# Performance work log

Hardware: AMD Instinct MI355X
Metric: run time of the kernel (lower is better)

The kernel has to match this reference:

```python
import jax, jax.numpy as jnp
import numpy as np

B, S, IN, D, H, K, NLVL = 8, 1536, 32, 128, 4, 7, 2
DFF = 4 * D
DK = D // H
EPS = 1e-6


def setup_inputs() -> dict:
    key = jax.random.key(0)
    ks = jax.random.split(key, 24)
    rn = lambda k, sh, s=0.05: jax.random.normal(k, sh, jnp.float32) * s
    z = lambda sh: jnp.zeros(sh, jnp.float32)
    o = lambda sh: jnp.ones(sh, jnp.float32)
    return {
        'x': jax.random.normal(ks[0], (B, S, IN), jnp.float32),
        'enc_W': rn(ks[1], (IN, D)), 'enc_b': z((D,)),
        'ln_rnn_a': o((NLVL, D)), 'ln_rnn_b': z((NLVL, D)),
        'gru_Wih': rn(ks[2], (NLVL, 3 * D, D)), 'gru_Whh': rn(ks[3], (NLVL, 3 * D, D)),
        'gru_bih': z((NLVL, 3 * D)), 'gru_bhh': z((NLVL, 3 * D)),
        'ln_attn_a': o((NLVL, D)), 'ln_attn_b': z((NLVL, D)),
        'Wq': rn(ks[4], (NLVL, D, D)), 'bq': z((NLVL, D)),
        'Wk': rn(ks[5], (NLVL, D, D)), 'bk': z((NLVL, D)),
        'Wv': rn(ks[6], (NLVL, D, D)), 'bv': z((NLVL, D)),
        'Wo': rn(ks[7], (NLVL, D, D)), 'bo': z((NLVL, D)),
        'ln_ff_a': o((NLVL, D)), 'ln_ff_b': z((NLVL, D)),
        'ff_W1': rn(ks[8], (NLVL, D, DFF)), 'ff_b1': z((NLVL, DFF)),
        'ff_W2': rn(ks[9], (NLVL, DFF, D)), 'ff_b2': z((NLVL, D)),
        'out_W': rn(ks[10], (D, 1)), 'out_b': z((1,)),
    }


def layernorm(x, a, b):
    # faithful to torch code: unbiased std (ddof=1), divide by (std + eps)
    m = x.mean(-1, keepdims=True)
    s = jnp.std(x, axis=-1, ddof=1, keepdims=True)
    return a * (x - m) / (s + EPS) + b


def local_rnn(x, Wih, Whh, bih, bhh):
    # x: [B,S,D]. Window each position into its ksize-length causal window,
    # run a GRU over the window (scan over K steps, batched over B*S), keep last h.
    xp = jnp.pad(x, ((0, 0), (K - 1, 0), (0, 0)))            # zero left-pad
    win = jnp.stack([xp[:, i:i + S] for i in range(K)], 0)   # [K,B,S,D]

    def step(h, xt):
        gi = xt @ Wih.T + bih                                 # [B,S,3D]
        gh = h @ Whh.T + bhh
        ir, iz, inn = jnp.split(gi, 3, -1)
        hr, hz, hn = jnp.split(gh, 3, -1)
        r = jax.nn.sigmoid(ir + hr)
        zz = jax.nn.sigmoid(iz + hz)
        nn_ = jnp.tanh(inn + r * hn)
        return (1.0 - zz) * nn_ + zz * h, None

    h, _ = jax.lax.scan(step, jnp.zeros_like(x), win)
    return h


def mhpool(x, Wq, bq, Wk, bk, Wv, bv, Wo, bo):
    def heads(w, bb):
        return jnp.swapaxes((x @ w + bb).reshape(B, S, H, DK), 1, 2)  # [B,H,S,DK]
    q, k, v = heads(Wq, bq), heads(Wk, bk), heads(Wv, bv)
    scores = jnp.einsum('bhqd,bhkd->bhqk', q, k) / np.float32(np.sqrt(DK))
    mask = jnp.tril(jnp.ones((S, S), bool))
    scores = jnp.where(mask, scores, jnp.float32(-1e9))
    p = jax.nn.softmax(scores, axis=-1)
    o = jnp.einsum('bhqk,bhkd->bhqd', p, v)
    o = jnp.swapaxes(o, 1, 2).reshape(B, S, D)
    return o @ Wo + bo


def reference(x, enc_W, enc_b, ln_rnn_a, ln_rnn_b, gru_Wih, gru_Whh, gru_bih,
              gru_bhh, ln_attn_a, ln_attn_b, Wq, bq, Wk, bk, Wv, bv, Wo, bo,
              ln_ff_a, ln_ff_b, ff_W1, ff_b1, ff_W2, ff_b2, out_W, out_b):
    h = x @ enc_W + enc_b
    for i in range(NLVL):
        # LocalRNNLayer (pre-norm residual); LocalRNN.output Linear is unused in orig forward
        h = h + local_rnn(layernorm(h, ln_rnn_a[i], ln_rnn_b[i]),
                          gru_Wih[i], gru_Whh[i], gru_bih[i], gru_bhh[i])
        # MHPooling sublayer
        h = h + mhpool(layernorm(h, ln_attn_a[i], ln_attn_b[i]),
                       Wq[i], bq[i], Wk[i], bk[i], Wv[i], bv[i], Wo[i], bo[i])
        # PositionwiseFeedForward sublayer
        hn = layernorm(h, ln_ff_a[i], ln_ff_b[i])
        h = h + (jax.nn.relu(hn @ ff_W1[i] + ff_b1[i]) @ ff_W2[i] + ff_b2[i])
    return jax.nn.sigmoid(h @ out_W + out_b)
```

## Files before the change

kernel.cpp:

```cpp
#include <hip/hip_runtime.h>
#include <math.h>

#define DEV_INLINE __device__ __forceinline__

constexpr int B = 8, S = 1536, IN = 32, D = 128, NH = 4, KWIN = 7, NLVL = 2;
constexpr int DFF = 512, DKH = 32;
constexpr int M = B * S;
constexpr int MD = M * D;
constexpr float EPS = 1e-6f;

typedef unsigned short u16;
typedef __bf16 bf16x8 __attribute__((ext_vector_type(8)));
typedef float f32x4 __attribute__((ext_vector_type(4)));
typedef unsigned short u16x4 __attribute__((ext_vector_type(4)));

#define MFMA16(a, b, c) __builtin_amdgcn_mfma_f32_16x16x32_bf16(a, b, c, 0, 0, 0)

DEV_INLINE float sigmoidf_(float x) { return 1.f / (1.f + __expf(-x)); }

DEV_INLINE u16 f2bf(float f) {
    unsigned u = __builtin_bit_cast(unsigned, f);
    unsigned rnd = 0x7FFFu + ((u >> 16) & 1u);
    return (u16)((u + rnd) >> 16);
}
// ... 18 lines not shown
__global__ void k_prep(const float* __restrict__ Wih, const float* __restrict__ Whh,
                       const float* __restrict__ Wq, const float* __restrict__ Wk,
                       const float* __restrict__ Wv, const float* __restrict__ Wo,
                       const float* __restrict__ W1, const float* __restrict__ W2,
                       u16* __restrict__ Wih16, u16* __restrict__ Whh16,
                       u16* __restrict__ Wqkv, u16* __restrict__ WoT,
                       u16* __restrict__ W1T, u16* __restrict__ W2T) {
    constexpr int SZ_GRU = NLVL * 384 * 128;
    constexpr int SZ_DD  = NLVL * 128 * 128;
    constexpr int SZ_FF  = NLVL * 128 * 512;
    int i = blockIdx.x * 256 + threadIdx.x;
    if (i < SZ_GRU) { Wih16[i] = f2bf(Wih[i]); return; }
    i -= SZ_GRU;
    if (i < SZ_GRU) { Whh16[i] = f2bf(Whh[i]); return; }
    i -= SZ_GRU;
    if (i < 3 * SZ_DD) {
        int seg = i / SZ_DD, j = i - seg * SZ_DD;
        int lvl = j >> 14, rem = j & 16383, k = rem >> 7, n = rem & 127;
        const float* src = seg == 0 ? Wq : (seg == 1 ? Wk : Wv);
        Wqkv[(size_t)lvl * 384 * 128 + (size_t)(seg * 128 + n) * 128 + k] = f2bf(src[j]);
        return;
    }
    i -= 3 * SZ_DD;
    if (i < SZ_DD) {
        int lvl = i >> 14, rem = i & 16383, k = rem >> 7, n = rem & 127;
        WoT[(size_t)lvl * 16384 + n * 128 + k] = f2bf(Wo[i]); return;
    }
    i -= SZ_DD;
    if (i < SZ_FF) {
        int lvl = i >> 16, rem = i & 65535, k = rem >> 9, n = rem & 511;
        W1T[(size_t)lvl * 65536 + n * 128 + k] = f2bf(W1[i]); return;
    }
    i -= SZ_FF;
    if (i < SZ_FF) {
        int lvl = i >> 16, rem = i & 65535, k = rem >> 7, n = rem & 127;
        W2T[(size_t)lvl * 65536 + n * 512 + k] = f2bf(W2[i]); return;
    }
}

__global__ __launch_bounds__(256) void k_encoder(
    const float* __restrict__ x, const float* __restrict__ W, const float* __restrict__ b,
    const float* __restrict__ ga, const float* __restrict__ gb,
    float* __restrict__ h, u16* __restrict__ xnout) {
    __shared__ float xs[32][33];
    __shared__ float Ws[32][128];
    const int tid = threadIdx.x;
    const int row0 = blockIdx.x * 32;
    for (int i = tid; i < 32 * 32; i += 256) xs[i >> 5][i & 31] = x[(size_t)row0 * IN + i];
    for (int i = tid; i < 32 * 128; i += 256) Ws[i >> 7][i & 127] = W[i];
    __syncthreads();
    const int r = tid >> 3, cg = (tid & 7) * 16;
    float acc[16];
    #pragma unroll
    for (int j = 0; j < 16; ++j) acc[j] = b[cg + j];
    for (int k = 0; k < IN; ++k) {
        const float xv = xs[r][k];
        #pragma unroll
        for (int j = 0; j < 16; ++j) acc[j] = fmaf(xv, Ws[k][cg + j], acc[j]);
    }
    float s = 0.f;
    #pragma unroll
    for (int j = 0; j < 16; ++j) s += acc[j];
    s += __shfl_xor(s, 1); s += __shfl_xor(s, 2); s += __shfl_xor(s, 4);
    const float mean = s * (1.f / D);
    float q = 0.f;
    #pragma unroll
    for (int j = 0; j < 16; ++j) { float d = acc[j] - mean; q += d * d; }
    q += __shfl_xor(q, 1); q += __shfl_xor(q, 2); q += __shfl_xor(q, 4);
    const float inv = 1.f / (sqrtf(q * (1.f / (D - 1))) + EPS);
    float* hp = h + (size_t)(row0 + r) * D + cg;
    u16* xp = xnout + (size_t)(row0 + r) * D + cg;
    #pragma unroll
    for (int jj = 0; jj < 4; ++jj) {
        float4 hv = make_float4(acc[4 * jj], acc[4 * jj + 1], acc[4 * jj + 2], acc[4 * jj + 3]);
        *(float4*)(hp + 4 * jj) = hv;
        u16x4 o;
        #pragma unroll
        for (int c = 0; c < 4; ++c)
            o[c] = f2bf(ga[cg + 4 * jj + c] * (acc[4 * jj + c] - mean) * inv + gb[cg + 4 * jj + c]);
        *(u16x4*)(xp + 4 * jj) = o;
    }
}

template <int KDIM>
__global__ __launch_bounds__(256) void k_gemm_mfma(
    const u16* __restrict__ A, const u16* __restrict__ Bt,
    const float* __restrict__ bias, u16* __restrict__ o16, int Ncols) {
    const int wave = threadIdx.x >> 6, lane = threadIdx.x & 63;
    const int col16 = lane & 15, quad = lane >> 4;
    const int row0 = (blockIdx.x * 4 + wave) * 32;
    const int c0 = blockIdx.y * 32;
    const u16* a0p = A + (size_t)(row0 + col16) * KDIM + quad * 8;
    const u16* b0p = Bt + (size_t)(c0 + col16) * KDIM + quad * 8;
    f32x4 acc00 = {0.f, 0.f, 0.f, 0.f}, acc01 = acc00, acc10 = acc00, acc11 = acc00;
    mfma_tile32<KDIM>(a0p, a0p + 16 * KDIM, b0p, b0p + 16 * KDIM, acc00, acc01, acc10, acc11);
    const float bv0 = bias ? bias[c0 + col16] : 0.f;
    const float bv1 = bias ? bias[c0 + 16 + col16] : 0.f;
    #pragma unroll
    for (int r = 0; r < 4; ++r) {
        const size_t r0 = (size_t)(row0 + quad * 4 + r) * Ncols;
        const size_t r1 = r0 + (size_t)16 * Ncols;
        o16[r0 + c0 + col16]      = f2bf(acc00[r] + bv0);
        o16[r0 + c0 + 16 + col16] = f2bf(acc01[r] + bv1);
        o16[r1 + c0 + col16]      = f2bf(acc10[r] + bv0);
        o16[r1 + c0 + 16 + col16] = f2bf(acc11[r] + bv1);
    }
}

__global__ __launch_bounds__(256) void k_gemm_qkv(
    const u16* __restrict__ A, const u16* __restrict__ Bqkv,
    const float* __restrict__ bq, const float* __restrict__ bk, const float* __restrict__ bv,
    u16* __restrict__ q16, u16* __restrict__ k16, u16* __restrict__ vt16) {
    constexpr float QS = 0.17677669529663687f * 1.4426950408889634f;
    const int wave = threadIdx.x >> 6, lane = threadIdx.x & 63;
    const int col16 = lane & 15, quad = lane >> 4;
    const int row0 = (blockIdx.x * 4 + wave) * 32;
    const int seg = blockIdx.y >> 2;
    const int c0 = (blockIdx.y & 3) * 32;
    const u16* a0p = A + (size_t)(row0 + col16) * 128 + quad * 8;
    const u16* b0p = Bqkv + (size_t)(seg * 128 + c0 + col16) * 128 + quad * 8;
    f32x4 acc00 = {0.f, 0.f, 0.f, 0.f}, acc01 = acc00, acc10 = acc00, acc11 = acc00;
    mfma_tile32<128>(a0p, a0p + 16 * 128, b0p, b0p + 16 * 128, acc00, acc01, acc10, acc11);
    const float* bias = seg == 0 ? bq : (seg == 1 ? bk : bv);
    const float bv0 = bias[c0 + col16];
    const float bv1 = bias[c0 + 16 + col16];
    if (seg < 2) {
        const float sc = seg == 0 ? QS : 1.f;
        u16* o16 = seg == 0 ? q16 : k16;
        #pragma unroll
        for (int r = 0; r < 4; ++r) {
            const size_t r0 = (size_t)(row0 + quad * 4 + r) * 128;
            const size_t r1 = r0 + 16 * 128;
            o16[r0 + c0 + col16]      = f2bf((acc00[r] + bv0) * sc);
            o16[r0 + c0 + 16 + col16] = f2bf((acc01[r] + bv1) * sc);
            o16[r1 + c0 + col16]      = f2bf((acc10[r] + bv0) * sc);
            o16[r1 + c0 + 16 + col16] = f2bf((acc11[r] + bv1) * sc);
        }
    } else {
        const int bb = row0 / S;
        const int ssv = row0 - bb * S;
        const int ca = c0 + col16, cb = c0 + 16 + col16;
        u16* pa = vt16 + ((size_t)((bb * NH + (ca >> 5)) * 32 + (ca & 31))) * S + ssv;
        u16* pb = vt16 + ((size_t)((bb * NH + (cb >> 5)) * 32 + (cb & 31))) * S + ssv;
        #pragma unroll
        for (int r = 0; r < 4; ++r) {
            const int lr = quad * 4 + r;
            pa[lr]      = f2bf(acc00[r] + bv0);
            pb[lr]      = f2bf(acc01[r] + bv1);
            pa[lr + 16] = f2bf(acc10[r] + bv0);
            pb[lr + 16] = f2bf(acc11[r] + bv1);
        }
    }
}

template <int KDIM>
__global__ __launch_bounds__(256) void k_gemm_row(
    const u16* __restrict__ A, const u16* __restrict__ Bt,
    const float* __restrict__ bias, float* __restrict__ hio,
    const float* __restrict__ ga, const float* __restrict__ gb,
    u16* __restrict__ xnout) {
    __shared__ float hL[32][132];
    const int wave = threadIdx.x >> 6, lane = threadIdx.x & 63;
    const int col16 = lane & 15, quad = lane >> 4;
    const int row0 = blockIdx.x * 32;
    const int c0 = wave * 32;
    const u16* a0p = A + (size_t)(row0 + col16) * KDIM + quad * 8;
    const u16* b0p = Bt + (size_t)(c0 + col16) * KDIM + quad * 8;
    f32x4 acc00 = {0.f, 0.f, 0.f, 0.f}, acc01 = acc00, acc10 = acc00, acc11 = acc00;
    mfma_tile32<KDIM>(a0p, a0p + 16 * KDIM, b0p, b0p + 16 * KDIM, acc00, acc01, acc10, acc11);
    const float bv0 = bias[c0 + col16];
    const float bv1 = bias[c0 + 16 + col16];
    #pragma unroll
    for (int r = 0; r < 4; ++r) {
        const int l0 = quad * 4 + r, l1 = 16 + quad * 4 + r;
        const size_t g0 = (size_t)(row0 + l0) * D, g1 = (size_t)(row0 + l1) * D;
        float v00 = acc00[r] + bv0 + hio[g0 + c0 + col16];
        float v01 = acc01[r] + bv1 + hio[g0 + c0 + 16 + col16];
        float v10 = acc10[r] + bv0 + hio[g1 + c0 + col16];
        float v11 = acc11[r] + bv1 + hio[g1 + c0 + 16 + col16];
        hio[g0 + c0 + col16]      = v00;  hL[l0][c0 + col16]      = v00;
        hio[g0 + c0 + 16 + col16] = v01;  hL[l0][c0 + 16 + col16] = v01;
        hio[g1 + c0 + col16]      = v10;  hL[l1][c0 + col16]      = v10;
        hio[g1 + c0 + 16 + col16] = v11;  hL[l1][c0 + 16 + col16] = v11;
    }
    __syncthreads();
    const int r = threadIdx.x >> 3, cg = (threadIdx.x & 7) * 16;
    float vals[16];
    #pragma unroll
    for (int jj = 0; jj < 4; ++jj) {
        float4 v = *(const float4*)&hL[r][cg + 4 * jj];
        vals[4 * jj] = v.x; vals[4 * jj + 1] = v.y; vals[4 * jj + 2] = v.z; vals[4 * jj + 3] = v.w;
    }
    float s = 0.f;
    #pragma unroll
    for (int j = 0; j < 16; ++j) s += vals[j];
    s += __shfl_xor(s, 1); s += __shfl_xor(s, 2); s += __shfl_xor(s, 4);
    const float mean = s * (1.f / D);
    float q = 0.f;
    #pragma unroll
    for (int j = 0; j < 16; ++j) { float d = vals[j] - mean; q += d * d; }
    q += __shfl_xor(q, 1); q += __shfl_xor(q, 2); q += __shfl_xor(q, 4);
    const float inv = 1.f / (sqrtf(q * (1.f / (D - 1))) + EPS);
    u16* xp = xnout + (size_t)(row0 + r) * D + cg;
    #pragma unroll
    for (int jj = 0; jj < 4; ++jj) {
        u16x4 o;
        #pragma unroll
        for (int c = 0; c < 4; ++c)
            o[c] = f2bf(ga[cg + 4 * jj + c] * (vals[4 * jj + c] - mean) * inv + gb[cg + 4 * jj + c]);
        *(u16x4*)(xp + 4 * jj) = o;
    }
}

template <bool LAST>
__global__ __launch_bounds__(256) void k_ffn(
    const u16* __restrict__ A, const u16* __restrict__ W1T, const float* __restrict__ b1,
    const u16* __restrict__ W2T, const float* __restrict__ b2, float* __restrict__ hio,
    const float* __restrict__ ga, const float* __restrict__ gb, u16* __restrict__ xnout,
    const float* __restrict__ outW, const float* __restrict__ outb, float* __restrict__ outp) {
    __shared__ __align__(16) u16 Ls[32][520];
    const int tid = threadIdx.x;
    const int wave = tid >> 6, lane = tid & 63;
    const int col16 = lane & 15, quad = lane >> 4;
    const int row0 = blockIdx.x * 32;
    const u16* a0p = A + (size_t)(row0 + col16) * 128 + quad * 8;
    const u16* a1p = a0p + 16 * 128;

    #pragma unroll
    for (int ct = 0; ct < 4; ++ct) {
        const int c0 = wave * 128 + ct * 32;
        const u16* b0p = W1T + (size_t)(c0 + col16) * 128 + quad * 8;
        f32x4 acc00 = {0.f, 0.f, 0.f, 0.f}, acc01 = acc00, acc10 = acc00, acc11 = acc00;
        mfma_tile32<128>(a0p, a1p, b0p, b0p + 16 * 128, acc00, acc01, acc10, acc11);
        const float bv0 = b1[c0 + col16];
        const float bv1 = b1[c0 + 16 + col16];
        #pragma unroll
        for (int r = 0; r < 4; ++r) {
            const int l0 = quad * 4 + r, l1 = 16 + quad * 4 + r;
            Ls[l0][c0 + col16]      = f2bf(fmaxf(acc00[r] + bv0, 0.f));
            Ls[l0][c0 + 16 + col16] = f2bf(fmaxf(acc01[r] + bv1, 0.f));
            Ls[l1][c0 + col16]      = f2bf(fmaxf(acc10[r] + bv0, 0.f));
            Ls[l1][c0 + 16 + col16] = f2bf(fmaxf(acc11[r] + bv1, 0.f));
        }
    }
    __syncthreads();

    const int c0 = wave * 32;
    f32x4 acc00 = {0.f, 0.f, 0.f, 0.f}, acc01 = acc00, acc10 = acc00, acc11 = acc00;
    #pragma unroll
    for (int k0 = 0; k0 < 512; k0 += 32) {
        bf16x8 a0 = *(const bf16x8*)&Ls[col16][k0 + quad * 8];
        bf16x8 a1 = *(const bf16x8*)&Ls[16 + col16][k0 + quad * 8];
        const u16* bp = W2T + (size_t)(c0 + col16) * 512 + k0 + quad * 8;
        bf16x8 b0 = *(const bf16x8*)bp;
        bf16x8 b1v = *(const bf16x8*)(bp + 16 * 512);
        acc00 = MFMA16(a0, b0, acc00);
        acc01 = MFMA16(a0, b1v, acc01);
        acc10 = MFMA16(a1, b0, acc10);
        acc11 = MFMA16(a1, b1v, acc11);
    }
    __syncthreads();
    float* hL = (float*)Ls;
    const float bv0 = b2[c0 + col16];
    const float bv1 = b2[c0 + 16 + col16];
    #pragma unroll
    for (int r = 0; r < 4; ++r) {
        const int l0 = quad * 4 + r, l1 = 16 + quad * 4 + r;
        const size_t g0 = (size_t)(row0 + l0) * D, g1 = (size_t)(row0 + l1) * D;
        float v00 = acc00[r] + bv0 + hio[g0 + c0 + col16];
        float v01 = acc01[r] + bv1 + hio[g0 + c0 + 16 + col16];
        float v10 = acc10[r] + bv0 + hio[g1 + c0 + col16];
        float v11 = acc11[r] + bv1 + hio[g1 + c0 + 16 + col16];
        hio[g0 + c0 + col16]      = v00;  hL[l0 * 132 + c0 + col16]      = v00;
        hio[g0 + c0 + 16 + col16] = v01;  hL[l0 * 132 + c0 + 16 + col16] = v01;
        hio[g1 + c0 + col16]      = v10;  hL[l1 * 132 + c0 + col16]      = v10;
        hio[g1 + c0 + 16 + col16] = v11;  hL[l1 * 132 + c0 + 16 + col16] = v11;
    }
    __syncthreads();
    const int r = tid >> 3, cg = (tid & 7) * 16;
    float vals[16];
    #pragma unroll
    for (int jj = 0; jj < 4; ++jj) {
        float4 v = *(const float4*)&hL[r * 132 + cg + 4 * jj];
        vals[4 * jj] = v.x; vals[4 * jj + 1] = v.y; vals[4 * jj + 2] = v.z; vals[4 * jj + 3] = v.w;
    }
    if constexpr (LAST) {
        float dot = 0.f;
        #pragma unroll
        for (int j = 0; j < 16; ++j) dot += vals[j] * outW[cg + j];
        dot += __shfl_xor(dot, 1); dot += __shfl_xor(dot, 2); dot += __shfl_xor(dot, 4);
        if ((tid & 7) == 0) outp[row0 + r] = sigmoidf_(dot + outb[0]);
    } else {
        float s = 0.f;
        #pragma unroll
        for (int j = 0; j < 16; ++j) s += vals[j];
        s += __shfl_xor(s, 1); s += __shfl_xor(s, 2); s += __shfl_xor(s, 4);
        const float mean = s * (1.f / D);
        float q = 0.f;
        #pragma unroll
        for (int j = 0; j < 16; ++j) { float d = vals[j] - mean; q += d * d; }
        q += __shfl_xor(q, 1); q += __shfl_xor(q, 2); q += __shfl_xor(q, 4);
        const float inv = 1.f / (sqrtf(q * (1.f / (D - 1))) + EPS);
        u16* xp = xnout + (size_t)(row0 + r) * D + cg;
        #pragma unroll
        for (int jj = 0; jj < 4; ++jj) {
            u16x4 o;
            #pragma unroll
            for (int c = 0; c < 4; ++c)
                o[c] = f2bf(ga[cg + 4 * jj + c] * (vals[4 * jj + c] - mean) * inv + gb[cg + 4 * jj + c]);
            *(u16x4*)(xp + 4 * jj) = o;
        }
    }
}

__global__ __launch_bounds__(512, 2) void k_gru_fused(
    const u16* __restrict__ Gb,
    const u16* __restrict__ Whh16,
    const float* __restrict__ bih, const float* __restrict__ bhh,
    float* __restrict__ hout,
    const float* __restrict__ ga, const float* __restrict__ gb,
    u16* __restrict__ xnout) {
    constexpr int RB = 48;
    __shared__ __align__(16) u16 Gs[(RB + 6) * 392];
    __shared__ __align__(16) u16 hs16[RB * 136];
    const int tid = threadIdx.x;
    const int wave = tid >> 6, lane = tid & 63;
    const int col16 = lane & 15, quad = lane >> 4;
    const int row0 = blockIdx.x * RB;
    const int ss0 = row0 % S;
    const int cc = wave * 16 + col16;

    for (int i = tid; i < (RB + 6) * 48; i += 512) {
        const int r = i / 48, c8 = (i - r * 48) * 8;
        bf16x8 val = {};
        if (ss0 - 6 + r >= 0)
            val = *(const bf16x8*)(Gb + (size_t)(row0 - 6 + r) * 384 + c8);
        *(bf16x8*)&Gs[r * 392 + c8] = val;
    }
    bf16x8 Breg[3][4];
    #pragma unroll
    for (int g = 0; g < 3; ++g)
        #pragma unroll
        for (int kc = 0; kc < 4; ++kc)
            Breg[g][kc] = *(const bf16x8*)(Whh16 + (size_t)(g * 128 + cc) * 128 + kc * 32 + quad * 8);
    float bi[3], bh[3];
    #pragma unroll
    for (int g = 0; g < 3; ++g) { bi[g] = bih[g * 128 + cc]; bh[g] = bhh[g * 128 + cc]; }
    float hp[12] = {};
    __syncthreads();

    for (int t = 0; t < KWIN; ++t) {
        const int shift = KWIN - 1 - t;
        f32x4 acc[3][3];
        #pragma unroll
        for (int rh = 0; rh < 3; ++rh)
            #pragma unroll
            for (int g = 0; g < 3; ++g) acc[rh][g] = {0.f, 0.f, 0.f, 0.f};
        if (t > 0) {
            bf16x8 af[3][4];
            #pragma unroll
            for (int rh = 0; rh < 3; ++rh)
                #pragma unroll
                for (int kc = 0; kc < 4; ++kc)
                    af[rh][kc] = *(const bf16x8*)&hs16[(rh * 16 + col16) * 136 + kc * 32 + quad * 8];
            __syncthreads();
            #pragma unroll
            for (int kc = 0; kc < 4; ++kc)
                #pragma unroll
                for (int g = 0; g < 3; ++g)
                    #pragma unroll
                    for (int rh = 0; rh < 3; ++rh)
                        acc[rh][g] = MFMA16(af[rh][kc], Breg[g][kc], acc[rh][g]);
        }
        const bool last = (t == KWIN - 1);
        #pragma unroll
        for (int rh = 0; rh < 3; ++rh) {
            #pragma unroll
            for (int r = 0; r < 4; ++r) {
                const int idx = rh * 4 + r;
                const int lrow = rh * 16 + quad * 4 + r;
                const int gr = lrow - shift + 6;
                float xr = 0.f, xz = 0.f, xn_ = 0.f;
                if (ss0 + lrow - shift >= 0) {
                    xr  = b2f(Gs[gr * 392 + cc]);
                    xz  = b2f(Gs[gr * 392 + 128 + cc]);
                    xn_ = b2f(Gs[gr * 392 + 256 + cc]);
                }
                const float rr = sigmoidf_(xr + bi[0] + acc[rh][0][r] + bh[0]);
                const float zz = sigmoidf_(xz + bi[1] + acc[rh][1][r] + bh[1]);
                const float e2 = __expf(2.f * (xn_ + bi[2] + rr * (acc[rh][2][r] + bh[2])));
                const float nn = 1.f - 2.f / (e2 + 1.f);
                const float hnew = (1.f - zz) * nn + zz * hp[idx];
                hp[idx] = hnew;
                if (!last) hs16[lrow * 136 + cc] = f2bf(hnew);
            }
        }
        __syncthreads();
    }
    float* hf = (float*)Gs;
    #pragma unroll
    for (int rh = 0; rh < 3; ++rh)
        #pragma unroll
        for (int r = 0; r < 4; ++r) {
            const int lrow = rh * 16 + quad * 4 + r;
            const float hv = hp[rh * 4 + r] + hout[(size_t)(row0 + lrow) * D + cc];
            hout[(size_t)(row0 + lrow) * D + cc] = hv;
            hf[lrow * 132 + cc] = hv;
        }
    __syncthreads();
    const int r = tid >> 3;
    if (r < RB) {
        const int cg = (tid & 7) * 16;
        float vals[16];
        #pragma unroll
        for (int jj = 0; jj < 4; ++jj) {
            float4 v = *(const float4*)&hf[r * 132 + cg + 4 * jj];
            vals[4 * jj] = v.x; vals[4 * jj + 1] = v.y; vals[4 * jj + 2] = v.z; vals[4 * jj + 3] = v.w;
        }
        float s = 0.f;
        #pragma unroll
        for (int j = 0; j < 16; ++j) s += vals[j];
        s += __shfl_xor(s, 1); s += __shfl_xor(s, 2); s += __shfl_xor(s, 4);
        const float mean = s * (1.f / D);
        float q = 0.f;
        #pragma unroll
        for (int j = 0; j < 16; ++j) { float d = vals[j] - mean; q += d * d; }
        q += __shfl_xor(q, 1); q += __shfl_xor(q, 2); q += __shfl_xor(q, 4);
        const float inv = 1.f / (sqrtf(q * (1.f / (D - 1))) + EPS);
        u16* xp = xnout + (size_t)(row0 + r) * D + cg;
        #pragma unroll
        for (int jj = 0; jj < 4; ++jj) {
            u16x4 o;
            #pragma unroll
            for (int c = 0; c < 4; ++c)
                o[c] = f2bf(ga[cg + 4 * jj + c] * (vals[4 * jj + c] - mean) * inv + gb[cg + 4 * jj + c]);
            *(u16x4*)(xp + 4 * jj) = o;
        }
    }
}

__global__ __launch_bounds__(256) void k_attn_mfma(
    const u16* __restrict__ Qb, const u16* __restrict__ Kb,
    const u16* __restrict__ Vt, u16* __restrict__ O16) {
    const int wave = threadIdx.x >> 6, lane = threadIdx.x & 63;
    const int p = blockIdx.x;
    const int bh = blockIdx.y;
    const int b = bh >> 2, hh = bh & 3;
    const int col = lane & 15, quad = lane >> 4;

    __shared__ __align__(16) u16 Pb[4][32][40];
    __shared__ float Om[4][32][33];
    __shared__ float Lm[4][32];
    u16 (* __restrict__ P)[40] = Pb[wave];

    const u16* Kbase = Kb + (size_t)b * S * 128 + hh * 32;
    const u16* Vbase = Vt + (size_t)bh * 32 * S;

    #pragma unroll
    for (int half = 0; half < 2; ++half) {
        const int qt = half == 0 ? p : 47 - p;
        const int q0 = qt * 32;
        const int nkt = qt + 1;
        const u16* qp = Qb + (size_t)(b * S + q0 + col) * 128 + hh * 32 + quad * 8;
        const bf16x8 qf0 = *(const bf16x8*)qp;
        const bf16x8 qf1 = *(const bf16x8*)(qp + 16 * 128);
        f32x4 o00 = {0.f, 0.f, 0.f, 0.f}, o01 = o00, o10 = o00, o11 = o00;
        float lsum[8] = {};
        int kt = wave;
        bf16x8 kf0 = {}, kf1 = {}, vf0 = {}, vf1 = {};
        if (kt < nkt) {
            const u16* kp = Kbase + (size_t)(kt * 32 + col) * 128 + quad * 8;
            kf0 = *(const bf16x8*)kp;
            kf1 = *(const bf16x8*)(kp + 16 * 128);
            const u16* vp = Vbase + (size_t)col * S + kt * 32 + quad * 8;
            vf0 = *(const bf16x8*)vp;
            vf1 = *(const bf16x8*)(vp + 16 * S);
        }
        while (kt < nkt) {
            const int ktn = kt + 4;
            bf16x8 nk0 = kf0, nk1 = kf1, nv0 = vf0, nv1 = vf1;
            if (ktn < nkt) {
                const u16* kp = Kbase + (size_t)(ktn * 32 + col) * 128 + quad * 8;
                nk0 = *(const bf16x8*)kp;
                nk1 = *(const bf16x8*)(kp + 16 * 128);
                const u16* vp = Vbase + (size_t)col * S + ktn * 32 + quad * 8;
                nv0 = *(const bf16x8*)vp;
                nv1 = *(const bf16x8*)(vp + 16 * S);
            }
            f32x4 z = {0.f, 0.f, 0.f, 0.f};
            f32x4 s00 = MFMA16(qf0, kf0, z);
            f32x4 s01 = MFMA16(qf0, kf1, z);
            f32x4 s10 = MFMA16(qf1, kf0, z);
            f32x4 s11 = MFMA16(qf1, kf1, z);
            const bool diag = (kt == qt);
            const int k0g = kt * 32;
            #pragma unroll
            for (int r = 0; r < 4; ++r) {
                const int lr = quad * 4 + r;
                float p00 = __builtin_amdgcn_exp2f(s00[r]);
                float p01 = __builtin_amdgcn_exp2f(s01[r]);
                float p10 = __builtin_amdgcn_exp2f(s10[r]);
                float p11 = __builtin_amdgcn_exp2f(s11[r]);
                if (diag) {
                    const int qg0 = q0 + lr, qg1 = q0 + 16 + lr;
                    if (k0g + col > qg0)      p00 = 0.f;
                    if (k0g + 16 + col > qg0) p01 = 0.f;
                    if (k0g + col > qg1)      p10 = 0.f;
                    if (k0g + 16 + col > qg1) p11 = 0.f;
                }
                lsum[r]     += p00 + p01;
                lsum[4 + r] += p10 + p11;
                P[lr][col]           = f2bf(p00);
                P[lr][16 + col]      = f2bf(p01);
                P[16 + lr][col]      = f2bf(p10);
                P[16 + lr][16 + col] = f2bf(p11);
            }
            const bf16x8 pa0 = *(const bf16x8*)&P[col][quad * 8];
            const bf16x8 pa1 = *(const bf16x8*)&P[16 + col][quad * 8];
            o00 = MFMA16(pa0, vf0, o00);
            o01 = MFMA16(pa0, vf1, o01);
            o10 = MFMA16(pa1, vf0, o10);
            o11 = MFMA16(pa1, vf1, o11);
            kf0 = nk0; kf1 = nk1; vf0 = nv0; vf1 = nv1;
            kt = ktn;
        }
        #pragma unroll
        for (int i = 0; i < 8; ++i) {
            float v = lsum[i];
            v += __shfl_xor(v, 1); v += __shfl_xor(v, 2);
            v += __shfl_xor(v, 4); v += __shfl_xor(v, 8);
            lsum[i] = v;
        }
        #pragma unroll
        for (int r = 0; r < 4; ++r) {
            const int lr = quad * 4 + r;
            Om[wave][lr][col]           = o00[r];
            Om[wave][lr][16 + col]      = o01[r];
            Om[wave][16 + lr][col]      = o10[r];
            Om[wave][16 + lr][16 + col] = o11[r];
        }
        if (col == 0) {
            #pragma unroll
            for (int i = 0; i < 8; ++i)
                Lm[wave][(i >> 2) * 16 + quad * 4 + (i & 3)] = lsum[i];
        }
        __syncthreads();
        {
            const int tr = threadIdx.x >> 3, tc = (threadIdx.x & 7) * 4;
            const float inv = 1.f / (Lm[0][tr] + Lm[1][tr] + Lm[2][tr] + Lm[3][tr]);
            u16x4 outv;
            #pragma unroll
            for (int c = 0; c < 4; ++c) {
                const float o = Om[0][tr][tc + c] + Om[1][tr][tc + c] +
                                Om[2][tr][tc + c] + Om[3][tr][tc + c];
                outv[c] = f2bf(o * inv);
            }
            *(u16x4*)(O16 + (size_t)(b * S + q0 + tr) * 128 + hh * 32 + tc) = outv;
        }
        __syncthreads();
    }
}

extern "C" void kernel_launch(void* const* d_in, const int* in_sizes, int n_in,
                              void* d_out, int out_size, void* d_ws, size_t ws_size,
                              hipStream_t stream) {
    const float* x       = (const float*)d_in[0];
    const float* enc_W   = (const float*)d_in[1];
    const float* enc_b   = (const float*)d_in[2];
    const float* ln_rnn_a = (const float*)d_in[3];
    const float* ln_rnn_b = (const float*)d_in[4];
    const float* gru_Wih = (const float*)d_in[5];
    const float* gru_Whh = (const float*)d_in[6];
    const float* gru_bih = (const float*)d_in[7];
    const float* gru_bhh = (const float*)d_in[8];
    const float* ln_attn_a = (const float*)d_in[9];
    const float* ln_attn_b = (const float*)d_in[10];
    const float* Wq = (const float*)d_in[11];
    const float* bq = (const float*)d_in[12];
    const float* Wk = (const float*)d_in[13];
    const float* bk = (const float*)d_in[14];
    const float* Wv = (const float*)d_in[15];
    const float* bv = (const float*)d_in[16];
    const float* Wo = (const float*)d_in[17];
    const float* bo = (const float*)d_in[18];
    const float* ln_ff_a = (const float*)d_in[19];
    const float* ln_ff_b = (const float*)d_in[20];
    const float* ff_W1 = (const float*)d_in[21];
    const float* ff_b1 = (const float*)d_in[22];
    const float* ff_W2 = (const float*)d_in[23];
    const float* ff_b2 = (const float*)d_in[24];
    const float* out_W = (const float*)d_in[25];
    const float* out_b = (const float*)d_in[26];

    float* h   = (float*)d_ws;
    u16* pool  = (u16*)(h + MD);
    u16* xn16  = pool + (size_t)4 * MD;
    u16* Wih16 = xn16 + MD;
    u16* Whh16 = Wih16 + NLVL * 384 * D;
    u16* Wqkv  = Whh16 + NLVL * 384 * D;
    u16* WoT   = Wqkv + NLVL * 384 * D;
    u16* W1T   = WoT + NLVL * D * D;
    u16* W2T   = W1T + NLVL * D * DFF;

    u16* q16  = pool;
    u16* k16  = pool + MD;
    u16* vt16 = pool + (size_t)2 * MD;
    u16* ao16 = pool + (size_t)3 * MD;
    u16* G16  = pool;

    k_prep<<<2304, 256, 0, stream>>>(gru_Wih, gru_Whh, Wq, Wk, Wv, Wo, ff_W1, ff_W2,
                                     Wih16, Whh16, Wqkv, WoT, W1T, W2T);
    k_encoder<<<M / 32, 256, 0, stream>>>(x, enc_W, enc_b, ln_rnn_a, ln_rnn_b, h, xn16);

    for (int lvl = 0; lvl < NLVL; ++lvl) {
        k_gemm_mfma<128><<<dim3(96, 12), 256, 0, stream>>>(
            xn16, Wih16 + lvl * 384 * D, nullptr, G16, 384);
        k_gru_fused<<<256, 512, 0, stream>>>(
            G16, Whh16 + lvl * 384 * D, gru_bih + lvl * 384, gru_bhh + lvl * 384,
            h, ln_attn_a + lvl * D, ln_attn_b + lvl * D, xn16);

        k_gemm_qkv<<<dim3(96, 12), 256, 0, stream>>>(
            xn16, Wqkv + lvl * 384 * D, bq + lvl * D, bk + lvl * D, bv + lvl * D,
            q16, k16, vt16);
        k_attn_mfma<<<dim3(24, 32), 256, 0, stream>>>(q16, k16, vt16, ao16);
        k_gemm_row<128><<<M / 32, 256, 0, stream>>>(
            ao16, WoT + lvl * D * D, bo + lvl * D, h,
            ln_ff_a + lvl * D, ln_ff_b + lvl * D, xn16);

        if (lvl + 1 < NLVL) {
            k_ffn<false><<<M / 32, 256, 0, stream>>>(
                xn16, W1T + lvl * D * DFF, ff_b1 + lvl * DFF,
                W2T + lvl * DFF * D, ff_b2 + lvl * D, h,
                ln_rnn_a + (lvl + 1) * D, ln_rnn_b + (lvl + 1) * D, xn16,
                nullptr, nullptr, nullptr);
        } else {
            k_ffn<true><<<M / 32, 256, 0, stream>>>(
                xn16, W1T + lvl * D * DFF, ff_b1 + lvl * DFF,
                W2T + lvl * DFF * D, ff_b2 + lvl * D, h,
                nullptr, nullptr, nullptr,
                out_W, out_b, (float*)d_out);
        }
    }
}
```

Measured before the change: 360.0 us.

## Fuse GRU input projection into GRU kernel and merge Wo with FFN

The separate Wih GEMM is folded into the GRU kernel. Each block loads its normalized input rows plus a 16-row halo into shared memory and computes the gate preactivations with MFMA there, so the G buffer no longer round-trips through global memory. The output projection with its residual and LayerNorm is merged into the FFN kernel, and the intermediate h stays in shared memory instead of being written and reread. This removes two launches per level and several full-tensor passes through global memory, at the cost of redundant halo GEMM work and more shared memory per block, which may lower occupancy.

```diff
diff --git a/kernel.cpp b/kernel.cpp
--- a/kernel.cpp
+++ b/kernel.cpp
@@ -124,31 +124,6 @@
     }
 }
 
-template <int KDIM>
-__global__ __launch_bounds__(256) void k_gemm_mfma(
-    const u16* __restrict__ A, const u16* __restrict__ Bt,
-    const float* __restrict__ bias, u16* __restrict__ o16, int Ncols) {
-    const int wave = threadIdx.x >> 6, lane = threadIdx.x & 63;
-    const int col16 = lane & 15, quad = lane >> 4;
-    const int row0 = (blockIdx.x * 4 + wave) * 32;
-    const int c0 = blockIdx.y * 32;
-    const u16* a0p = A + (size_t)(row0 + col16) * KDIM + quad * 8;
-    const u16* b0p = Bt + (size_t)(c0 + col16) * KDIM + quad * 8;
-    f32x4 acc00 = {0.f, 0.f, 0.f, 0.f}, acc01 = acc00, acc10 = acc00, acc11 = acc00;
-    mfma_tile32<KDIM>(a0p, a0p + 16 * KDIM, b0p, b0p + 16 * KDIM, acc00, acc01, acc10, acc11);
-    const float bv0 = bias ? bias[c0 + col16] : 0.f;
-    const float bv1 = bias ? bias[c0 + 16 + col16] : 0.f;
-    #pragma unroll
-    for (int r = 0; r < 4; ++r) {
-        const size_t r0 = (size_t)(row0 + quad * 4 + r) * Ncols;
-        const size_t r1 = r0 + (size_t)16 * Ncols;
-        o16[r0 + c0 + col16]      = f2bf(acc00[r] + bv0);
-        o16[r0 + c0 + 16 + col16] = f2bf(acc01[r] + bv1);
-        o16[r1 + c0 + col16]      = f2bf(acc10[r] + bv0);
-        o16[r1 + c0 + 16 + col16] = f2bf(acc11[r] + bv1);
-    }
-}
-
 __global__ __launch_bounds__(256) void k_gemm_qkv(
     const u16* __restrict__ A, const u16* __restrict__ Bqkv,
     const float* __restrict__ bq, const float* __restrict__ bk, const float* __restrict__ bv,
@@ -195,175 +170,17 @@
     }
 }
 
-template <int KDIM>
-__global__ __launch_bounds__(256) void k_gemm_row(
-    const u16* __restrict__ A, const u16* __restrict__ Bt,
-    const float* __restrict__ bias, float* __restrict__ hio,
-    const float* __restrict__ ga, const float* __restrict__ gb,
-    u16* __restrict__ xnout) {
-    __shared__ float hL[32][132];
-    const int wave = threadIdx.x >> 6, lane = threadIdx.x & 63;
-    const int col16 = lane & 15, quad = lane >> 4;
-    const int row0 = blockIdx.x * 32;
-    const int c0 = wave * 32;
-    const u16* a0p = A + (size_t)(row0 + col16) * KDIM + quad * 8;
-    const u16* b0p = Bt + (size_t)(c0 + col16) * KDIM + quad * 8;
-    f32x4 acc00 = {0.f, 0.f, 0.f, 0.f}, acc01 = acc00, acc10 = acc00, acc11 = acc00;
-    mfma_tile32<KDIM>(a0p, a0p + 16 * KDIM, b0p, b0p + 16 * KDIM, acc00, acc01, acc10, acc11);
-    const float bv0 = bias[c0 + col16];
-    const float bv1 = bias[c0 + 16 + col16];
-    #pragma unroll
-    for (int r = 0; r < 4; ++r) {
-        const int l0 = quad * 4 + r, l1 = 16 + quad * 4 + r;
-        const size_t g0 = (size_t)(row0 + l0) * D, g1 = (size_t)(row0 + l1) * D;
-        float v00 = acc00[r] + bv0 + hio[g0 + c0 + col16];
-        float v01 = acc01[r] + bv1 + hio[g0 + c0 + 16 + col16];
-        float v10 = acc10[r] + bv0 + hio[g1 + c0 + col16];
-        float v11 = acc11[r] + bv1 + hio[g1 + c0 + 16 + col16];
-        hio[g0 + c0 + col16]      = v00;  hL[l0][c0 + col16]      = v00;
-        hio[g0 + c0 + 16 + col16] = v01;  hL[l0][c0 + 16 + col16] = v01;
-        hio[g1 + c0 + col16]      = v10;  hL[l1][c0 + col16]      = v10;
-        hio[g1 + c0 + 16 + col16] = v11;  hL[l1][c0 + 16 + col16] = v11;
-    }
-    __syncthreads();
-    const int r = threadIdx.x >> 3, cg = (threadIdx.x & 7) * 16;
-    float vals[16];
-    #pragma unroll
-    for (int jj = 0; jj < 4; ++jj) {
-        float4 v = *(const float4*)&hL[r][cg + 4 * jj];
-        vals[4 * jj] = v.x; vals[4 * jj + 1] = v.y; vals[4 * jj + 2] = v.z; vals[4 * jj + 3] = v.w;
-    }
-    float s = 0.f;
-    #pragma unroll
-    for (int j = 0; j < 16; ++j) s += vals[j];
-    s += __shfl_xor(s, 1); s += __shfl_xor(s, 2); s += __shfl_xor(s, 4);
-    const float mean = s * (1.f / D);
-    float q = 0.f;
-    #pragma unroll
-    for (int j = 0; j < 16; ++j) { float d = vals[j] - mean; q += d * d; }
-    q += __shfl_xor(q, 1); q += __shfl_xor(q, 2); q += __shfl_xor(q, 4);
-    const float inv = 1.f / (sqrtf(q * (1.f / (D - 1))) + EPS);
-    u16* xp = xnout + (size_t)(row0 + r) * D + cg;
-    #pragma unroll
-    for (int jj = 0; jj < 4; ++jj) {
-        u16x4 o;
-        #pragma unroll
-        for (int c = 0; c < 4; ++c)
-            o[c] = f2bf(ga[cg + 4 * jj + c] * (vals[4 * jj + c] - mean) * inv + gb[cg + 4 * jj + c]);
-        *(u16x4*)(xp + 4 * jj) = o;
-    }
-}
-
-template <bool LAST>
-__global__ __launch_bounds__(256) void k_ffn(
-    const u16* __restrict__ A, const u16* __restrict__ W1T, const float* __restrict__ b1,
-    const u16* __restrict__ W2T, const float* __restrict__ b2, float* __restrict__ hio,
-    const float* __restrict__ ga, const float* __restrict__ gb, u16* __restrict__ xnout,
-    const float* __restrict__ outW, const float* __restrict__ outb, float* __restrict__ outp) {
-    __shared__ __align__(16) u16 Ls[32][520];
-    const int tid = threadIdx.x;
-    const int wave = tid >> 6, lane = tid & 63;
-    const int col16 = lane & 15, quad = lane >> 4;
-    const int row0 = blockIdx.x * 32;
-    const u16* a0p = A + (size_t)(row0 + col16) * 128 + quad * 8;
-    const u16* a1p = a0p + 16 * 128;
-
-    #pragma unroll
-    for (int ct = 0; ct < 4; ++ct) {
-        const int c0 = wave * 128 + ct * 32;
-        const u16* b0p = W1T + (size_t)(c0 + col16) * 128 + quad * 8;
-        f32x4 acc00 = {0.f, 0.f, 0.f, 0.f}, acc01 = acc00, acc10 = acc00, acc11 = acc00;
-        mfma_tile32<128>(a0p, a1p, b0p, b0p + 16 * 128, acc00, acc01, acc10, acc11);
-        const float bv0 = b1[c0 + col16];
-        const float bv1 = b1[c0 + 16 + col16];
-        #pragma unroll
-        for (int r = 0; r < 4; ++r) {
-            const int l0 = quad * 4 + r, l1 = 16 + quad * 4 + r;
-            Ls[l0][c0 + col16]      = f2bf(fmaxf(acc00[r] + bv0, 0.f));
-            Ls[l0][c0 + 16 + col16] = f2bf(fmaxf(acc01[r] + bv1, 0.f));
-            Ls[l1][c0 + col16]      = f2bf(fmaxf(acc10[r] + bv0, 0.f));
-            Ls[l1][c0 + 16 + col16] = f2bf(fmaxf(acc11[r] + bv1, 0.f));
-        }
-    }
-    __syncthreads();
-
-    const int c0 = wave * 32;
-    f32x4 acc00 = {0.f, 0.f, 0.f, 0.f}, acc01 = acc00, acc10 = acc00, acc11 = acc00;
-    #pragma unroll
-    for (int k0 = 0; k0 < 512; k0 += 32) {
-        bf16x8 a0 = *(const bf16x8*)&Ls[col16][k0 + quad * 8];
-        bf16x8 a1 = *(const bf16x8*)&Ls[16 + col16][k0 + quad * 8];
-        const u16* bp = W2T + (size_t)(c0 + col16) * 512 + k0 + quad * 8;
-        bf16x8 b0 = *(const bf16x8*)bp;
-        bf16x8 b1v = *(const bf16x8*)(bp + 16 * 512);
-        acc00 = MFMA16(a0, b0, acc00);
-        acc01 = MFMA16(a0, b1v, acc01);
-        acc10 = MFMA16(a1, b0, acc10);
-        acc11 = MFMA16(a1, b1v, acc11);
-    }
-    __syncthreads();
-    float* hL = (float*)Ls;
-    const float bv0 = b2[c0 + col16];
-    const float bv1 = b2[c0 + 16 + col16];
-    #pragma unroll
-    for (int r = 0; r < 4; ++r) {
-        const int l0 = quad * 4 + r, l1 = 16 + quad * 4 + r;
-        const size_t g0 = (size_t)(row0 + l0) * D, g1 = (size_t)(row0 + l1) * D;
-        float v00 = acc00[r] + bv0 + hio[g0 + c0 + col16];
-        float v01 = acc01[r] + bv1 + hio[g0 + c0 + 16 + col16];
-        float v10 = acc10[r] + bv0 + hio[g1 + c0 + col16];
-        float v11 = acc11[r] + bv1 + hio[g1 + c0 + 16 + col16];
-        hio[g0 + c0 + col16]      = v00;  hL[l0 * 132 + c0 + col16]      = v00;
-        hio[g0 + c0 + 16 + col16] = v01;  hL[l0 * 132 + c0 + 16 + col16] = v01;
-        hio[g1 + c0 + col16]      = v10;  hL[l1 * 132 + c0 + col16]      = v10;
-        hio[g1 + c0 + 16 + col16] = v11;  hL[l1 * 132 + c0 + 16 + col16] = v11;
-    }
-    __syncthreads();
-    const int r = tid >> 3, cg = (tid & 7) * 16;
-    float vals[16];
-    #pragma unroll
-    for (int jj = 0; jj < 4; ++jj) {
-        float4 v = *(const float4*)&hL[r * 132 + cg + 4 * jj];
-        vals[4 * jj] = v.x; vals[4 * jj + 1] = v.y; vals[4 * jj + 2] = v.z; vals[4 * jj + 3] = v.w;
-    }
-    if constexpr (LAST) {
-        float dot = 0.f;
-        #pragma unroll
-        for (int j = 0; j < 16; ++j) dot += vals[j] * outW[cg + j];
-        dot += __shfl_xor(dot, 1); dot += __shfl_xor(dot, 2); dot += __shfl_xor(dot, 4);
-        if ((tid & 7) == 0) outp[row0 + r] = sigmoidf_(dot + outb[0]);
-    } else {
-        float s = 0.f;
-        #pragma unroll
-        for (int j = 0; j < 16; ++j) s += vals[j];
-        s += __shfl_xor(s, 1); s += __shfl_xor(s, 2); s += __shfl_xor(s, 4);
-        const float mean = s * (1.f / D);
-        float q = 0.f;
-        #pragma unroll
-        for (int j = 0; j < 16; ++j) { float d = vals[j] - mean; q += d * d; }
-        q += __shfl_xor(q, 1); q += __shfl_xor(q, 2); q += __shfl_xor(q, 4);
-        const float inv = 1.f / (sqrtf(q * (1.f / (D - 1))) + EPS);
-        u16* xp = xnout + (size_t)(row0 + r) * D + cg;
-        #pragma unroll
-        for (int jj = 0; jj < 4; ++jj) {
-            u16x4 o;
-            #pragma unroll
-            for (int c = 0; c < 4; ++c)
-                o[c] = f2bf(ga[cg + 4 * jj + c] * (vals[4 * jj + c] - mean) * inv + gb[cg + 4 * jj + c]);
-            *(u16x4*)(xp + 4 * jj) = o;
-        }
-    }
-}
-
 __global__ __launch_bounds__(512, 2) void k_gru_fused(
-    const u16* __restrict__ Gb,
+    const u16* __restrict__ xn,
+    const u16* __restrict__ Wih16,
     const u16* __restrict__ Whh16,
     const float* __restrict__ bih, const float* __restrict__ bhh,
     float* __restrict__ hout,
     const float* __restrict__ ga, const float* __restrict__ gb,
-    u16* __restrict__ xnout) {
+    u16* __restrict__ xnaout) {
     constexpr int RB = 48;
-    __shared__ __align__(16) u16 Gs[(RB + 6) * 392];
+    __shared__ __align__(16) u16 xnS[64 * 136];
+    __shared__ __align__(16) u16 Gs[64 * 392];
     __shared__ __align__(16) u16 hs16[RB * 136];
     const int tid = threadIdx.x;
     const int wave = tid >> 6, lane = tid & 63;
@@ -372,12 +189,12 @@
     const int ss0 = row0 % S;
     const int cc = wave * 16 + col16;
 
-    for (int i = tid; i < (RB + 6) * 48; i += 512) {
-        const int r = i / 48, c8 = (i - r * 48) * 8;
+    for (int i = tid; i < 64 * 16; i += 512) {
+        const int r = i >> 4, c8 = (i & 15) * 8;
         bf16x8 val = {};
-        if (ss0 - 6 + r >= 0)
-            val = *(const bf16x8*)(Gb + (size_t)(row0 - 6 + r) * 384 + c8);
-        *(bf16x8*)&Gs[r * 392 + c8] = val;
+        if (ss0 - 16 + r >= 0)
+            val = *(const bf16x8*)(xn + (size_t)(row0 - 16 + r) * 128 + c8);
+        *(bf16x8*)&xnS[r * 136 + c8] = val;
     }
     bf16x8 Breg[3][4];
     #pragma unroll
@@ -388,6 +205,33 @@
     float bi[3], bh[3];
     #pragma unroll
     for (int g = 0; g < 3; ++g) { bi[g] = bih[g * 128 + cc]; bh[g] = bhh[g * 128 + cc]; }
+    __syncthreads();
+
+    #pragma unroll
+    for (int tt = wave; tt < 24; tt += 8) {
+        const int rt = tt / 12, ct = tt - rt * 12;
+        const u16* bp = Wih16 + (size_t)(ct * 32 + col16) * 128 + quad * 8;
+        f32x4 a00 = {0.f, 0.f, 0.f, 0.f}, a01 = a00, a10 = a00, a11 = a00;
+        #pragma unroll
+        for (int k0 = 0; k0 < 128; k0 += 32) {
+            bf16x8 af0 = *(const bf16x8*)&xnS[(rt * 32 + col16) * 136 + k0 + quad * 8];
+            bf16x8 af1 = *(const bf16x8*)&xnS[(rt * 32 + 16 + col16) * 136 + k0 + quad * 8];
+            bf16x8 b0 = *(const bf16x8*)(bp + k0);
+            bf16x8 b1 = *(const bf16x8*)(bp + 16 * 128 + k0);
+            a00 = MFMA16(af0, b0, a00);
+            a01 = MFMA16(af0, b1, a01);
+            a10 = MFMA16(af1, b0, a10);
+            a11 = MFMA16(af1, b1, a11);
+        }
+        #pragma unroll
+        for (int r = 0; r < 4; ++r) {
+            const int gr0 = rt * 32 + quad * 4 + r, gr1 = gr0 + 16;
+            Gs[gr0 * 392 + ct * 32 + col16]      = f2bf(a00[r]);
+            Gs[gr0 * 392 + ct * 32 + 16 + col16] = f2bf(a01[r]);
+            Gs[gr1 * 392 + ct * 32 + col16]      = f2bf(a10[r]);
+            Gs[gr1 * 392 + ct * 32 + 16 + col16] = f2bf(a11[r]);
+        }
+    }
     float hp[12] = {};
     __syncthreads();
 
@@ -421,13 +265,10 @@
             for (int r = 0; r < 4; ++r) {
                 const int idx = rh * 4 + r;
                 const int lrow = rh * 16 + quad * 4 + r;
-                const int gr = lrow - shift + 6;
-                float xr = 0.f, xz = 0.f, xn_ = 0.f;
-                if (ss0 + lrow - shift >= 0) {
-                    xr  = b2f(Gs[gr * 392 + cc]);
-                    xz  = b2f(Gs[gr * 392 + 128 + cc]);
-                    xn_ = b2f(Gs[gr * 392 + 256 + cc]);
-                }
+                const int gr = lrow - shift + 16;
+                const float xr  = b2f(Gs[gr * 392 + cc]);
+                const float xz  = b2f(Gs[gr * 392 + 128 + cc]);
+                const float xn_ = b2f(Gs[gr * 392 + 256 + cc]);
                 const float rr = sigmoidf_(xr + bi[0] + acc[rh][0][r] + bh[0]);
                 const float zz = sigmoidf_(xz + bi[1] + acc[rh][1][r] + bh[1]);
                 const float e2 = __expf(2.f * (xn_ + bi[2] + rr * (acc[rh][2][r] + bh[2])));
@@ -469,7 +310,7 @@
         for (int j = 0; j < 16; ++j) { float d = vals[j] - mean; q += d * d; }
         q += __shfl_xor(q, 1); q += __shfl_xor(q, 2); q += __shfl_xor(q, 4);
         const float inv = 1.f / (sqrtf(q * (1.f / (D - 1))) + EPS);
-        u16* xp = xnout + (size_t)(row0 + r) * D + cg;
+        u16* xp = xnaout + (size_t)(row0 + r) * D + cg;
         #pragma unroll
         for (int jj = 0; jj < 4; ++jj) {
             u16x4 o;
@@ -482,8 +323,8 @@
 }
 
 __global__ __launch_bounds__(256) void k_attn_mfma(
-    const u16* __restrict__ Qb, const u16* __restrict__ Kb,
-    const u16* __restrict__ Vt, u16* __restrict__ O16) {
+    const u16* Qb, const u16* __restrict__ Kb,
+    const u16* __restrict__ Vt, u16* O16) {
     const int wave = threadIdx.x >> 6, lane = threadIdx.x & 63;
     const int p = blockIdx.x;
     const int bh = blockIdx.y;
@@ -600,6 +441,171 @@
             *(u16x4*)(O16 + (size_t)(b * S + q0 + tr) * 128 + hh * 32 + tc) = outv;
         }
         __syncthreads();
+    }
+}
+
+template <bool LAST>
+__global__ __launch_bounds__(256) void k_mho_ffn(
+    const u16* __restrict__ ao, const u16* __restrict__ WoT, const float* __restrict__ bo,
+    float* __restrict__ hio,
+    const float* __restrict__ ga1, const float* __restrict__ gb1,
+    const u16* __restrict__ W1T, const float* __restrict__ b1,
+    const u16* __restrict__ W2T, const float* __restrict__ b2,
+    const float* __restrict__ ga2, const float* __restrict__ gb2, u16* __restrict__ xnout,
+    const float* __restrict__ outW, const float* __restrict__ outb, float* __restrict__ outp) {
+    __shared__ float hL[32 * 132];
+    __shared__ __align__(16) u16 xnL[32 * 136];
+    __shared__ __align__(16) u16 Ls[32 * 520];
+    const int tid = threadIdx.x;
+    const int wave = tid >> 6, lane = tid & 63;
+    const int col16 = lane & 15, quad = lane >> 4;
+    const int row0 = blockIdx.x * 32;
+    const int c0 = wave * 32;
+
+    {
+        const u16* a0p = ao + (size_t)(row0 + col16) * 128 + quad * 8;
+        const u16* b0p = WoT + (size_t)(c0 + col16) * 128 + quad * 8;
+        f32x4 acc00 = {0.f, 0.f, 0.f, 0.f}, acc01 = acc00, acc10 = acc00, acc11 = acc00;
+        mfma_tile32<128>(a0p, a0p + 16 * 128, b0p, b0p + 16 * 128, acc00, acc01, acc10, acc11);
+        const float bv0 = bo[c0 + col16];
+        const float bv1 = bo[c0 + 16 + col16];
+        #pragma unroll
+        for (int r = 0; r < 4; ++r) {
+            const int l0 = quad * 4 + r, l1 = 16 + quad * 4 + r;
+            const size_t g0 = (size_t)(row0 + l0) * D, g1 = (size_t)(row0 + l1) * D;
+            hL[l0 * 132 + c0 + col16]      = acc00[r] + bv0 + hio[g0 + c0 + col16];
+            hL[l0 * 132 + c0 + 16 + col16] = acc01[r] + bv1 + hio[g0 + c0 + 16 + col16];
+            hL[l1 * 132 + c0 + col16]      = acc10[r] + bv0 + hio[g1 + c0 + col16];
+            hL[l1 * 132 + c0 + 16 + col16] = acc11[r] + bv1 + hio[g1 + c0 + 16 + col16];
+        }
+    }
+    __syncthreads();
+    {
+        const int r = tid >> 3, cg = (tid & 7) * 16;
+        float vals[16];
+        #pragma unroll
+        for (int jj = 0; jj < 4; ++jj) {
+            float4 v = *(const float4*)&hL[r * 132 + cg + 4 * jj];
+            vals[4 * jj] = v.x; vals[4 * jj + 1] = v.y; vals[4 * jj + 2] = v.z; vals[4 * jj + 3] = v.w;
+        }
+        float s = 0.f;
+        #pragma unroll
+        for (int j = 0; j < 16; ++j) s += vals[j];
+        s += __shfl_xor(s, 1); s += __shfl_xor(s, 2); s += __shfl_xor(s, 4);
+        const float mean = s * (1.f / D);
+        float q = 0.f;
+        #pragma unroll
+        for (int j = 0; j < 16; ++j) { float d = vals[j] - mean; q += d * d; }
+        q += __shfl_xor(q, 1); q += __shfl_xor(q, 2); q += __shfl_xor(q, 4);
+        const float inv = 1.f / (sqrtf(q * (1.f / (D - 1))) + EPS);
+        #pragma unroll
+        for (int jj = 0; jj < 4; ++jj) {
+            u16x4 o;
+            #pragma unroll
+            for (int c = 0; c < 4; ++c)
+                o[c] = f2bf(ga1[cg + 4 * jj + c] * (vals[4 * jj + c] - mean) * inv + gb1[cg + 4 * jj + c]);
+            *(u16x4*)&xnL[r * 136 + cg + 4 * jj] = o;
+        }
+    }
+    __syncthreads();
+    #pragma unroll
+    for (int ct = 0; ct < 4; ++ct) {
+        const int c0f = wave * 128 + ct * 32;
+        const u16* b0p = W1T + (size_t)(c0f + col16) * 128 + quad * 8;
+        f32x4 acc00 = {0.f, 0.f, 0.f, 0.f}, acc01 = acc00, acc10 = acc00, acc11 = acc00;
+        #pragma unroll
+        for (int k0 = 0; k0 < 128; k0 += 32) {
+            bf16x8 a0 = *(const bf16x8*)&xnL[col16 * 136 + k0 + quad * 8];
+            bf16x8 a1 = *(const bf16x8*)&xnL[(16 + col16) * 136 + k0 + quad * 8];
+            bf16x8 b0 = *(const bf16x8*)(b0p + k0);
+            bf16x8 b1 = *(const bf16x8*)(b0p + 16 * 128 + k0);
+            acc00 = MFMA16(a0, b0, acc00);
+            acc01 = MFMA16(a0, b1, acc01);
+            acc10 = MFMA16(a1, b0, acc10);
+            acc11 = MFMA16(a1, b1, acc11);
+        }
+        const float bv0 = b1[c0f + col16];
+        const float bv1 = b1[c0f + 16 + col16];
+        #pragma unroll
+        for (int r = 0; r < 4; ++r) {
+            const int l0 = quad * 4 + r, l1 = 16 + quad * 4 + r;
+            Ls[l0 * 520 + c0f + col16]      = f2bf(fmaxf(acc00[r] + bv0, 0.f));
+            Ls[l0 * 520 + c0f + 16 + col16] = f2bf(fmaxf(acc01[r] + bv1, 0.f));
+            Ls[l1 * 520 + c0f + col16]      = f2bf(fmaxf(acc10[r] + bv0, 0.f));
+            Ls[l1 * 520 + c0f + 16 + col16] = f2bf(fmaxf(acc11[r] + bv1, 0.f));
+        }
+    }
+    __syncthreads();
+    {
+        f32x4 acc00 = {0.f, 0.f, 0.f, 0.f}, acc01 = acc00, acc10 = acc00, acc11 = acc00;
+        #pragma unroll
+        for (int k0 = 0; k0 < 512; k0 += 32) {
+            bf16x8 a0 = *(const bf16x8*)&Ls[col16 * 520 + k0 + quad * 8];
+            bf16x8 a1 = *(const bf16x8*)&Ls[(16 + col16) * 520 + k0 + quad * 8];
+            const u16* bp = W2T + (size_t)(c0 + col16) * 512 + k0 + quad * 8;
+            bf16x8 b0 = *(const bf16x8*)bp;
+            bf16x8 b1v = *(const bf16x8*)(bp + 16 * 512);
+            acc00 = MFMA16(a0, b0, acc00);
+            acc01 = MFMA16(a0, b1v, acc01);
+            acc10 = MFMA16(a1, b0, acc10);
+            acc11 = MFMA16(a1, b1v, acc11);
+        }
+        const float bv0 = b2[c0 + col16];
+        const float bv1 = b2[c0 + 16 + col16];
+        #pragma unroll
+        for (int r = 0; r < 4; ++r) {
+            const int l0 = quad * 4 + r, l1 = 16 + quad * 4 + r;
+            const size_t g0 = (size_t)(row0 + l0) * D, g1 = (size_t)(row0 + l1) * D;
+            const float v00 = acc00[r] + bv0 + hL[l0 * 132 + c0 + col16];
+            const float v01 = acc01[r] + bv1 + hL[l0 * 132 + c0 + 16 + col16];
+            const float v10 = acc10[r] + bv0 + hL[l1 * 132 + c0 + col16];
+            const float v11 = acc11[r] + bv1 + hL[l1 * 132 + c0 + 16 + col16];
+            hio[g0 + c0 + col16]      = v00;
+            hio[g0 + c0 + 16 + col16] = v01;
+            hio[g1 + c0 + col16]      = v10;
+            hio[g1 + c0 + 16 + col16] = v11;
+            hL[l0 * 132 + c0 + col16]      = v00;
+            hL[l0 * 132 + c0 + 16 + col16] = v01;
+            hL[l1 * 132 + c0 + col16]      = v10;
+            hL[l1 * 132 + c0 + 16 + col16] = v11;
+        }
+    }
+    __syncthreads();
+    {
+        const int r = tid >> 3, cg = (tid & 7) * 16;
+        float vals[16];
+        #pragma unroll
+        for (int jj = 0; jj < 4; ++jj) {
+            float4 v = *(const float4*)&hL[r * 132 + cg + 4 * jj];
+            vals[4 * jj] = v.x; vals[4 * jj + 1] = v.y; vals[4 * jj + 2] = v.z; vals[4 * jj + 3] = v.w;
+        }
+        if constexpr (LAST) {
+            float dot = 0.f;
+            #pragma unroll
+            for (int j = 0; j < 16; ++j) dot += vals[j] * outW[cg + j];
+            dot += __shfl_xor(dot, 1); dot += __shfl_xor(dot, 2); dot += __shfl_xor(dot, 4);
+            if ((tid & 7) == 0) outp[row0 + r] = sigmoidf_(dot + outb[0]);
+        } else {
+            float s = 0.f;
+            #pragma unroll
+            for (int j = 0; j < 16; ++j) s += vals[j];
+            s += __shfl_xor(s, 1); s += __shfl_xor(s, 2); s += __shfl_xor(s, 4);
+            const float mean = s * (1.f / D);
+            float q = 0.f;
+            #pragma unroll
+            for (int j = 0; j < 16; ++j) { float d = vals[j] - mean; q += d * d; }
+            q += __shfl_xor(q, 1); q += __shfl_xor(q, 2); q += __shfl_xor(q, 4);
+            const float inv = 1.f / (sqrtf(q * (1.f / (D - 1))) + EPS);
+            u16* xp = xnout + (size_t)(row0 + r) * D + cg;
+            #pragma unroll
+            for (int jj = 0; jj < 4; ++jj) {
+                u16x4 o;
+                #pragma unroll
+                for (int c = 0; c < 4; ++c)
+                    o[c] = f2bf(ga2[cg + 4 * jj + c] * (vals[4 * jj + c] - mean) * inv + gb2[cg + 4 * jj + c]);
+                *(u16x4*)(xp + 4 * jj) = o;
+            }
+        }
     }
 }
 
@@ -644,41 +650,41 @@
     u16* W1T   = WoT + NLVL * D * D;
     u16* W2T   = W1T + NLVL * D * DFF;
 
-    u16* q16  = pool;
-    u16* k16  = pool + MD;
-    u16* vt16 = pool + (size_t)2 * MD;
-    u16* ao16 = pool + (size_t)3 * MD;
-    u16* G16  = pool;
+    u16* q16   = pool;
+    u16* k16   = pool + MD;
+    u16* vt16  = pool + (size_t)2 * MD;
+    u16* xna16 = pool + (size_t)3 * MD;
+    u16* ao16  = q16;
 
     k_prep<<<2304, 256, 0, stream>>>(gru_Wih, gru_Whh, Wq, Wk, Wv, Wo, ff_W1, ff_W2,
                                      Wih16, Whh16, Wqkv, WoT, W1T, W2T);
     k_encoder<<<M / 32, 256, 0, stream>>>(x, enc_W, enc_b, ln_rnn_a, ln_rnn_b, h, xn16);
 
     for (int lvl = 0; lvl < NLVL; ++lvl) {
-        k_gemm_mfma<128><<<dim3(96, 12), 256, 0, stream>>>(
-            xn16, Wih16 + lvl * 384 * D, nullptr, G16, 384);
         k_gru_fused<<<256, 512, 0, stream>>>(
-            G16, Whh16 + lvl * 384 * D, gru_bih + lvl * 384, gru_bhh + lvl * 384,
-            h, ln_attn_a + lvl * D, ln_attn_b + lvl * D, xn16);
+            xn16, Wih16 + lvl * 384 * D, Whh16 + lvl * 384 * D,
+            gru_bih + lvl * 384, gru_bhh + lvl * 384,
+            h, ln_attn_a + lvl * D, ln_attn_b + lvl * D, xna16);
 
         k_gemm_qkv<<<dim3(96, 12), 256, 0, stream>>>(
-            xn16, Wqkv + lvl * 384 * D, bq + lvl * D, bk + lvl * D, bv + lvl * D,
+            xna16, Wqkv + lvl * 384 * D, bq + lvl * D, bk + lvl * D, bv + lvl * D,
             q16, k16, vt16);
         k_attn_mfma<<<dim3(24, 32), 256, 0, stream>>>(q16, k16, vt16, ao16);
-        k_gemm_row<128><<<M / 32, 256, 0, stream>>>(
-            ao16, WoT + lvl * D * D, bo + lvl * D, h,
-            ln_ff_a + lvl * D, ln_ff_b + lvl * D, xn16);
 
         if (lvl + 1 < NLVL) {
-            k_ffn<false><<<M / 32, 256, 0, stream>>>(
-                xn16, W1T + lvl * D * DFF, ff_b1 + lvl * DFF,
-                W2T + lvl * DFF * D, ff_b2 + lvl * D, h,
+            k_mho_ffn<false><<<M / 32, 256, 0, stream>>>(
+                ao16, WoT + lvl * D * D, bo + lvl * D, h,
+                ln_ff_a + lvl * D, ln_ff_b + lvl * D,
+                W1T + lvl * D * DFF, ff_b1 + lvl * DFF,
+                W2T + lvl * DFF * D, ff_b2 + lvl * D,
                 ln_rnn_a + (lvl + 1) * D, ln_rnn_b + (lvl + 1) * D, xn16,
                 nullptr, nullptr, nullptr);
         } else {
-            k_ffn<true><<<M / 32, 256, 0, stream>>>(
-                xn16, W1T + lvl * D * DFF, ff_b1 + lvl * DFF,
-                W2T + lvl * DFF * D, ff_b2 + lvl * D, h,
+            k_mho_ffn<true><<<M / 32, 256, 0, stream>>>(
+                ao16, WoT + lvl * D * D, bo + lvl * D, h,
+                ln_ff_a + lvl * D, ln_ff_b + lvl * D,
+                W1T + lvl * D * DFF, ff_b1 + lvl * DFF,
+                W2T + lvl * DFF * D, ff_b2 + lvl * D,
                 nullptr, nullptr, nullptr,
                 out_W, out_b, (float*)d_out);
         }
```

New measurement: 322.7 us. 1.12x faster.
